# Optimization experiments

Hardware: AMD Instinct MI355X
Metric: run time of the kernel (lower is better)

Reference implementation:

```python
import jax, jax.numpy as jnp
import numpy as np

S, B, D, H, DFF = 1024, 8, 1024, 16, 4096
HD = D // H
EPS = 1e-5


def layernorm(x, g, b):
    m = jnp.mean(x, axis=-1, keepdims=True)
    v = jnp.mean(jnp.square(x - m), axis=-1, keepdims=True)
    return (x - m) * jax.lax.rsqrt(v + EPS) * g + b


def setup_inputs() -> dict:
    key = jax.random.key(0)
    ks = jax.random.split(key, 6)
    w = 0.02
    return {
        "src": jax.random.normal(ks[0], (S, B, D), dtype=jnp.float32),
        "in_proj_w": jax.random.normal(ks[1], (3 * D, D), dtype=jnp.float32) * w,
        "in_proj_b": jnp.zeros((3 * D,), dtype=jnp.float32),
        "out_w": jax.random.normal(ks[2], (D, D), dtype=jnp.float32) * w,
        "out_b": jnp.zeros((D,), dtype=jnp.float32),
        "lin1_w": jax.random.normal(ks[3], (DFF, D), dtype=jnp.float32) * w,
        "lin1_b": jnp.zeros((DFF,), dtype=jnp.float32),
        "lin2_w": jax.random.normal(ks[4], (D, DFF), dtype=jnp.float32) * w,
        "lin2_b": jnp.zeros((D,), dtype=jnp.float32),
        "n1_g": jnp.ones((D,), dtype=jnp.float32),
        "n1_b": jnp.zeros((D,), dtype=jnp.float32),
        "n2_g": jnp.ones((D,), dtype=jnp.float32),
        "n2_b": jnp.zeros((D,), dtype=jnp.float32),
    }


def reference(src, in_proj_w, in_proj_b, out_w, out_b,
              lin1_w, lin1_b, lin2_w, lin2_b,
              n1_g, n1_b, n2_g, n2_b):
    # self-attention block (eval mode: dropout = identity)
    qkv = jnp.einsum('sbd,ed->sbe', src, in_proj_w) + in_proj_b  # [S,B,3D]
    q, k, v = jnp.split(qkv, 3, axis=-1)
    q = q.reshape(S, B, H, HD) * (1.0 / np.sqrt(HD)).astype(np.float32)
    k = k.reshape(S, B, H, HD)
    v = v.reshape(S, B, H, HD)
    scores = jnp.einsum('sbhd,tbhd->bhst', q, k)        # [B,H,S,S]
    attn = jax.nn.softmax(scores, axis=-1)
    o = jnp.einsum('bhst,tbhd->sbhd', attn, v).reshape(S, B, D)
    o = jnp.einsum('sbd,ed->sbe', o, out_w) + out_b
    # post-LN residuals
    x = layernorm(src + o, n1_g, n1_b)
    h = jax.nn.relu(jnp.einsum('sbd,fd->sbf', x, lin1_w) + lin1_b)
    f = jnp.einsum('sbf,df->sbd', h, lin2_w) + lin2_b
    return layernorm(x + f, n2_g, n2_b)
```

## Files before the change

### kernel.cpp

```cpp
#include <hip/hip_runtime.h>
#include <cstdint>
#include <cstddef>

#define S_  1024
#define B_  8
#define D_  1024
#define H_  16
#define HD_ 64
#define DFF_ 4096
#define M_  (S_*B_)
#define QKV_N (3*D_)

typedef float f32x4 __attribute__((ext_vector_type(4)));
typedef __bf16 bf16x8 __attribute__((ext_vector_type(8)));
typedef __bf16 bf16x4 __attribute__((ext_vector_type(4)));

#define GLDS16(gp, lp) __builtin_amdgcn_global_load_lds( \
    (__attribute__((address_space(1))) void*)(gp), \
    (__attribute__((address_space(3))) void*)(lp), 16, 0, 0)

#define CB0 (M_*D_/4)
#define CB1 (CB0 + QKV_N*D_/4)
#define CB2 (CB1 + D_*D_/4)
#define CB3 (CB2 + DFF_*D_/4)
#define CB4 (CB3 + D_*DFF_/4)

__global__ __launch_bounds__(256)
void cvt_all(const float* __restrict__ src, const float* __restrict__ w1f,
             const float* __restrict__ w2f, const float* __restrict__ w3f,
             const float* __restrict__ w4f,
             __bf16* __restrict__ src_bf, __bf16* __restrict__ w1,
             __bf16* __restrict__ w2, __bf16* __restrict__ w3,
             __bf16* __restrict__ w4)
{
    int i = blockIdx.x * 256 + threadIdx.x;
    const float* in; __bf16* out; int off;
    if      (i < CB0) { in = src; out = src_bf; off = 0;   }
    else if (i < CB1) { in = w1f; out = w1;     off = CB0; }
    else if (i < CB2) { in = w2f; out = w2;     off = CB1; }
    else if (i < CB3) { in = w3f; out = w3;     off = CB2; }
    else if (i < CB4) { in = w4f; out = w4;     off = CB3; }
    else return;
    int j = i - off;
    float4 v = *(const float4*)(in + (size_t)j * 4);
    __bf16 t[4] = {(__bf16)v.x, (__bf16)v.y, (__bf16)v.z, (__bf16)v.w};
    *(uint2*)(out + (size_t)j * 4) = *(uint2*)t;
}

template<bool OUT_BF16, bool RELU, bool ADD_BIAS, bool SPLITZ>
__global__ __launch_bounds__(512, 2)
void gemm256(const __bf16* __restrict__ A, const __bf16* __restrict__ W,
             const float* __restrict__ bias,
             void* __restrict__ Cv0, void* __restrict__ Cv1,
             int N, int Kloop, int lda)
{
    extern __shared__ __bf16 lds[];

    const int tid  = threadIdx.x;
    const int lane = tid & 63;
    const int wv   = tid >> 6;
    const int quad = lane >> 4;
    const int l15  = lane & 15;
    const int wm   = (wv >> 2) * 128;
    const int wn   = (wv & 3) * 64;

    const int id  = blockIdx.y * gridDim.x + blockIdx.x;
    const int nwg = gridDim.x * gridDim.y;
    const int q8  = nwg >> 3;
    const int k   = (id & 7) * q8 + (id >> 3);
    const int within = k & 31;
    const int chunk  = k >> 5;
    const int nchm   = gridDim.x >> 3;
    const int cm     = chunk % nchm;
    const int cn     = chunk / nchm;
    const int m0 = (cm * 8 + (within & 7)) * 256;
    const int n0 = (cn * 4 + (within >> 3)) * 256;

    void* Cv = Cv0;
    if (SPLITZ) {
        const int koff = blockIdx.z * Kloop;
        A += koff;
        W += koff;
        if (blockIdx.z) Cv = Cv1;
    }

    const int nt = Kloop >> 5;

    const int crow = tid >> 2;
    const int csl  = (tid & 3) ^ ((crow >> 1) & 3);
    const __bf16* gA0 = A + (size_t)(m0 + crow) * lda + csl * 8;
    const __bf16* gA1 = gA0 + (size_t)128 * lda;
    const __bf16* gW0 = W + (size_t)(n0 + crow) * lda + csl * 8;
    const __bf16* gW1 = gW0 + (size_t)128 * lda;
    char* ldsSt = (char*)lds + tid * 16;

    #define STAGE(kt, buf) do { \
        const int ko = (kt) << 5; \
        char* d_ = ldsSt + (buf) * 32768; \
        GLDS16(gW0 + ko, d_ + 16384); \
        GLDS16(gW1 + ko, d_ + 24576); \
        GLDS16(gA0 + ko, d_); \
        GLDS16(gA1 + ko, d_ + 8192); \
    } while (0)

    const int swz = (quad ^ ((l15 >> 1) & 3)) * 8;
    const __bf16* aBase = lds + (wm + l15) * 32 + swz;
    const __bf16* bBase = lds + 8192 + (wn + l15) * 32 + swz;

    #define RDA_ALL(arr, buf) do { const __bf16* p_ = aBase + (buf) * 16384; \
        _Pragma("unroll") for (int i_ = 0; i_ < 8; ++i_) \
            arr[i_] = *(const bf16x8*)(p_ + i_ * 512); } while (0)
    #define RDB_ALL(arr, buf) do { const __bf16* p_ = bBase + (buf) * 16384; \
        _Pragma("unroll") for (int j_ = 0; j_ < 4; ++j_) \
            arr[j_] = *(const bf16x8*)(p_ + j_ * 512); } while (0)

    #define BARRIER_DRAIN() do { \
        asm volatile("s_waitcnt vmcnt(0)" ::: "memory"); \
        __builtin_amdgcn_s_barrier(); \
        __builtin_amdgcn_sched_barrier(0); \
    } while (0)

    STAGE(0, 0);
    STAGE(1, 1);
    BARRIER_DRAIN();

    f32x4 acc[8][4] = {};
    bf16x8 aP[8], aN[8], b_[4];

    RDA_ALL(aP, 0);

    int b_cur = 0;
    for (int t = 0; t < nt; t += 2) {
        int b_nxt = b_cur + 1; if (b_nxt == 3) b_nxt = 0;
        int b_st  = b_nxt + 1; if (b_st  == 3) b_st  = 0;

        if (t + 2 < nt) STAGE(t + 2, b_st);
        RDB_ALL(b_, b_cur);
        RDA_ALL(aN, b_nxt);
        __builtin_amdgcn_s_setprio(1);
        #pragma unroll
        for (int i = 0; i < 8; ++i)
            #pragma unroll
            for (int j = 0; j < 4; ++j)
                acc[i][j] = __builtin_amdgcn_mfma_f32_16x16x32_bf16(aP[i], b_[j], acc[i][j], 0, 0, 0);
        __builtin_amdgcn_s_setprio(0);
        BARRIER_DRAIN();

        if (t + 3 < nt) STAGE(t + 3, b_cur);
        RDB_ALL(b_, b_nxt);
        if (t + 2 < nt) RDA_ALL(aP, b_st);
        __builtin_amdgcn_s_setprio(1);
        #pragma unroll
        for (int i = 0; i < 8; ++i)
            #pragma unroll
            for (int j = 0; j < 4; ++j)
                acc[i][j] = __builtin_amdgcn_mfma_f32_16x16x32_bf16(aN[i], b_[j], acc[i][j], 0, 0, 0);
        __builtin_amdgcn_s_setprio(0);
        if (t + 2 < nt) BARRIER_DRAIN();

        b_cur = b_st;
    }

    #undef BARRIER_DRAIN
    #undef RDA_ALL
    #undef RDB_ALL
    #undef STAGE

    float bvj[4];
    #pragma unroll
    for (int j = 0; j < 4; ++j)
        bvj[j] = ADD_BIAS ? bias[n0 + wn + j * 16 + l15] : 0.f;
    const size_t cbase = (size_t)(m0 + wm + quad * 4) * N + (n0 + wn + l15);
    #pragma unroll
    for (int i = 0; i < 8; ++i) {
        #pragma unroll
        for (int r = 0; r < 4; ++r) {
            const size_t rowb = cbase + (size_t)(i * 16 + r) * N;
            #pragma unroll
            for (int j = 0; j < 4; ++j) {
                float v = acc[i][j][r] + bvj[j];
                if (RELU) v = fmaxf(v, 0.f);
                if (OUT_BF16)
                    ((__bf16*)Cv)[rowb + j * 16] = (__bf16)v;
                else
                    ((float*)Cv)[rowb + j * 16] = v;
            }
        }
    }
}

template<bool OUT_BF16, bool RELU, bool ADD_BIAS, bool SPLITZ>
__global__ __launch_bounds__(512, 4)
void gemm128(const __bf16* __restrict__ A, const __bf16* __restrict__ W,
             const float* __restrict__ bias,
             void* __restrict__ Cv0, void* __restrict__ Cv1,
             int N, int Kloop, int lda)
{
    extern __shared__ __bf16 lds[];

    const int tid  = threadIdx.x;
    const int lane = tid & 63;
    const int wv   = tid >> 6;
    const int quad = lane >> 4;
    const int l15  = lane & 15;
    const int wm   = (wv & 1) * 64;
    const int wn   = (wv >> 1) * 64;

    const int id  = blockIdx.y * gridDim.x + blockIdx.x;
    const int nwg = gridDim.x * gridDim.y;
    const int q8  = nwg >> 3;
    const int k   = (id & 7) * q8 + (id >> 3);
    const int within = k & 31;
    const int chunk  = k >> 5;
    const int nchm   = gridDim.x >> 3;
    const int cm     = chunk % nchm;
    const int cn     = chunk / nchm;
    const int m0 = (cm * 8 + (within & 7)) * 128;
    const int n0 = (cn * 4 + (within >> 3)) * 256;

    void* Cv = Cv0;
    if (SPLITZ) {
        const int koff = blockIdx.z * Kloop;
        A += koff;
        W += koff;
        if (blockIdx.z) Cv = Cv1;
    }

    const int nt = Kloop >> 5;

    const int crow = tid >> 2;
    const int csl  = (tid & 3) ^ ((crow >> 1) & 3);
    const __bf16* gA0 = A + (size_t)(m0 + crow) * lda + csl * 8;
    const __bf16* gW0 = W + (size_t)(n0 + crow) * lda + csl * 8;
    const __bf16* gW1 = gW0 + (size_t)128 * lda;
    char* ldsSt = (char*)lds + tid * 16;

    #define STAGE(kt, buf) do { \
        const int ko = (kt) << 5; \
        char* d_ = ldsSt + (buf) * 24576; \
        GLDS16(gW0 + ko, d_ + 8192); \
        GLDS16(gW1 + ko, d_ + 16384); \
        GLDS16(gA0 + ko, d_); \
    } while (0)

    const int swz = (quad ^ ((l15 >> 1) & 3)) * 8;
    const __bf16* aBase = lds + (wm + l15) * 32 + swz;
    const __bf16* bBase = lds + 4096 + (wn + l15) * 32 + swz;

    #define BARRIER_DRAIN() do { \
        asm volatile("s_waitcnt vmcnt(0)" ::: "memory"); \
        __builtin_amdgcn_s_barrier(); \
        __builtin_amdgcn_sched_barrier(0); \
    } while (0)

    STAGE(0, 0);
    BARRIER_DRAIN();

    f32x4 acc[4][4] = {};

    for (int t = 0; t < nt; ++t) {
        const int cur = t & 1;
        if (t + 1 < nt) STAGE(t + 1, cur ^ 1);

        const __bf16* aB = aBase + cur * 12288;
        const __bf16* bB = bBase + cur * 12288;
        bf16x8 b_[4];
        #pragma unroll
        for (int j = 0; j < 4; ++j)
            b_[j] = *(const bf16x8*)(bB + j * 512);
        __builtin_amdgcn_s_setprio(1);
        #pragma unroll
        for (int i = 0; i < 4; ++i) {
            bf16x8 a_ = *(const bf16x8*)(aB + i * 512);
            #pragma unroll
            for (int j = 0; j < 4; ++j)
                acc[i][j] = __builtin_amdgcn_mfma_f32_16x16x32_bf16(a_, b_[j], acc[i][j], 0, 0, 0);
        }
        __builtin_amdgcn_s_setprio(0);

        if (t + 1 < nt) BARRIER_DRAIN();
    }

    #undef BARRIER_DRAIN
    #undef STAGE

    float bvj[4];
    #pragma unroll
    for (int j = 0; j < 4; ++j)
        bvj[j] = ADD_BIAS ? bias[n0 + wn + j * 16 + l15] : 0.f;
    const size_t cbase = (size_t)(m0 + wm + quad * 4) * N + (n0 + wn + l15);
    #pragma unroll
    for (int i = 0; i < 4; ++i) {
        #pragma unroll
        for (int r = 0; r < 4; ++r) {
            const size_t rowb = cbase + (size_t)(i * 16 + r) * N;
            #pragma unroll
            for (int j = 0; j < 4; ++j) {
                float v = acc[i][j][r] + bvj[j];
                if (RELU) v = fmaxf(v, 0.f);
                if (OUT_BF16)
                    ((__bf16*)Cv)[rowb + j * 16] = (__bf16)v;
                else
                    ((float*)Cv)[rowb + j * 16] = v;
            }
        }
    }
}

__global__ __launch_bounds__(256)
void v_transpose(const __bf16* __restrict__ qkv, __bf16* __restrict__ vt)
{
    __shared__ __bf16 T[64 * 65];
    const int tid = threadIdx.x;
    const int t0  = blockIdx.x * 64;
    const int bh  = blockIdx.y;
    const int b   = bh & (B_ - 1);
    const int h   = bh / B_;

    #pragma unroll
    for (int j = 0; j < 2; ++j) {
        int c = j * 256 + tid;
        int i = c >> 3, cc = c & 7;
        const __bf16* g = qkv + (size_t)((t0 + i) * B_ + b) * QKV_N + 2 * D_ + h * HD_ + cc * 8;
        bf16x8 v = *(const bf16x8*)g;
        #pragma unroll
        for (int u = 0; u < 8; ++u) T[(cc * 8 + u) * 65 + i] = v[u];
    }
    __syncthreads();
    #pragma unroll
    for (int j = 0; j < 2; ++j) {
        int c = j * 256 + tid;
        int d = c >> 3, cc = c & 7;
        __bf16 pk[8];
        #pragma unroll
        for (int u = 0; u < 8; ++u) pk[u] = T[d * 65 + cc * 8 + u];
        *(uint4*)(vt + ((size_t)bh * HD_ + d) * S_ + t0 + cc * 8) = *(uint4*)pk;
    }
}

__global__ __launch_bounds__(512, 4)
void attn_flash(const __bf16* __restrict__ qkv, const __bf16* __restrict__ vt,
                __bf16* __restrict__ out)
{
    extern __shared__ __bf16 alds[];
    __bf16* Ks0 = alds;
    __bf16* Vs0 = alds + 16384;
    __bf16* Ps  = alds + 32768;

    const int tid  = threadIdx.x;
    const int lane = tid & 63;
    const int wv   = tid >> 6;
    const int quad = lane >> 4;
    const int l15  = lane & 15;

    const int id = blockIdx.y * gridDim.x + blockIdx.x;
    const int k  = (id & 7) * ((S_ / 128) * B_ * H_ / 8) + (id >> 3);
    const int s0 = (k & 7) * 128;
    const int bh = k >> 3;
    const int b  = bh & (B_ - 1);
    const int h  = bh / B_;

    const int i0k = tid >> 3, cck = tid & 7, scck = cck ^ (i0k & 7);
    const int i0v = tid >> 4, ccv = tid & 15, sccv = ccv ^ (i0v & 15);
    const __bf16* gK0 = qkv + ((size_t)i0k * B_ + b) * QKV_N + D_ + h * HD_ + scck * 8;
    const __bf16* gK1 = gK0 + (size_t)64 * B_ * QKV_N;
    const __bf16* gV0 = vt + ((size_t)bh * HD_ + i0v) * S_ + sccv * 8;
    const __bf16* gV1 = gV0 + (size_t)32 * S_;
    char* dK = (char*)Ks0 + tid * 16;
    char* dV = (char*)Vs0 + tid * 16;
    const size_t KADV = (size_t)128 * B_ * QKV_N;

    #define STAGEKV(buf) do { \
        GLDS16(gK0, dK + (buf) * 16384); \
        GLDS16(gK1, dK + (buf) * 16384 + 8192); \
        GLDS16(gV0, dV + (buf) * 16384); \
        GLDS16(gV1, dV + (buf) * 16384 + 8192); \
        gK0 += KADV; gK1 += KADV; gV0 += 128; gV1 += 128; \
    } while (0)

    STAGEKV(0);

    const int qrow = wv * 16 + l15;
    bf16x8 bq[2];
    #pragma unroll
    for (int kk = 0; kk < 2; ++kk)
        bq[kk] = *(const bf16x8*)(qkv + (size_t)((s0 + qrow) * B_ + b) * QKV_N
                                  + h * HD_ + kk * 32 + quad * 8);

    __syncthreads();

    f32x4 oacc[4] = {};
    float l_run = 0.f;
    const float C2 = 0.125f * 1.44269504f;
    const int xk = l15 & 7;
    const __bf16* psB = Ps + qrow * 64;

    const int nt2 = S_ / 128;
    for (int it = 0; it < nt2; ++it) {
        const int cur = it & 1;
        if (it + 1 < nt2) STAGEKV(cur ^ 1);

        #pragma unroll
        for (int s = 0; s < 2; ++s) {
            f32x4 sacc[4] = {};
            #pragma unroll
            for (int kk = 0; kk < 2; ++kk) {
                const __bf16* akB = Ks0 + cur * 8192 + s * 4096 + l15 * 64
                                    + (((kk * 4 + quad) ^ xk) * 8);
                #pragma unroll
                for (int j = 0; j < 4; ++j)
                    sacc[j] = __builtin_amdgcn_mfma_f32_16x16x32_bf16(
                        *(const bf16x8*)(akB + j * 1024), bq[kk], sacc[j], 0, 0, 0);
            }

            float rs = 0.f;
            #pragma unroll
            for (int j = 0; j < 4; ++j)
                #pragma unroll
                for (int r = 0; r < 4; ++r) {
                    float p = __builtin_amdgcn_exp2f(sacc[j][r] * C2);
                    sacc[j][r] = p;
                    rs += p;
                }
            rs += __shfl_xor(rs, 16, 64);
            rs += __shfl_xor(rs, 32, 64);
            l_run += rs;

            #pragma unroll
            for (int j = 0; j < 4; ++j) {
                __bf16 pk[4] = {(__bf16)sacc[j][0], (__bf16)sacc[j][1],
                                (__bf16)sacc[j][2], (__bf16)sacc[j][3]};
                int s16 = (j * 2 + (quad >> 1)) ^ xk;
                *(uint2*)(psB + s16 * 8 + (quad & 1) * 4) = *(uint2*)pk;
            }

            #pragma unroll
            for (int kk = 0; kk < 2; ++kk) {
                bf16x8 ap = *(const bf16x8*)(psB + (((kk * 4 + quad) ^ xk) * 8));
                const __bf16* bvB = Vs0 + cur * 8192 + l15 * 128
                                    + (((s * 8 + kk * 4 + quad) ^ l15) * 8);
                #pragma unroll
                for (int jd = 0; jd < 4; ++jd)
                    oacc[jd] = __builtin_amdgcn_mfma_f32_16x16x32_bf16(
                        ap, *(const bf16x8*)(bvB + jd * 2048), oacc[jd], 0, 0, 0);
            }
        }

        __syncthreads();
    }
    #undef STAGEKV

    float linv = 1.f / l_run;
    #pragma unroll
    for (int r = 0; r < 4; ++r) {
        float lr = __shfl(linv, quad * 4 + r, 64);
        int s = s0 + wv * 16 + quad * 4 + r;
        #pragma unroll
        for (int jd = 0; jd < 4; ++jd) {
            int d = jd * 16 + l15;
            out[(size_t)(s * B_ + b) * D_ + h * HD_ + d] = (__bf16)(oacc[jd][r] * lr);
        }
    }
}

__global__ __launch_bounds__(256)
void ln_res3(const float* __restrict__ xa, const __bf16* __restrict__ p0,
             const __bf16* __restrict__ p1, const float* __restrict__ bias,
             const float* __restrict__ g, const float* __restrict__ beta,
             float* __restrict__ yout, __bf16* __restrict__ ybf)
{
    __shared__ float red[8];
    const int row = blockIdx.x;
    const int tid = threadIdx.x;
    const size_t base = (size_t)row * D_ + tid * 4;

    float4 a  = *(const float4*)(xa + base);
    bf16x4 q0 = *(const bf16x4*)(p0 + base);
    bf16x4 q1 = *(const bf16x4*)(p1 + base);
    float4 bb = *(const float4*)(bias + tid * 4);
    float x0 = a.x + (float)q0[0] + (float)q1[0] + bb.x;
    float x1 = a.y + (float)q0[1] + (float)q1[1] + bb.y;
    float x2 = a.z + (float)q0[2] + (float)q1[2] + bb.z;
    float x3 = a.w + (float)q0[3] + (float)q1[3] + bb.w;

    float s  = x0 + x1 + x2 + x3;
    float ss = x0 * x0 + x1 * x1 + x2 * x2 + x3 * x3;
    for (int msk = 1; msk <= 32; msk <<= 1) {
        s  += __shfl_xor(s,  msk, 64);
        ss += __shfl_xor(ss, msk, 64);
    }
    const int wv = tid >> 6;
    if ((tid & 63) == 0) { red[wv] = s; red[4 + wv] = ss; }
    __syncthreads();
    s  = red[0] + red[1] + red[2] + red[3];
    ss = red[4] + red[5] + red[6] + red[7];
    float mean = s * (1.f / D_);
    float var  = ss * (1.f / D_) - mean * mean;
    float rstd = rsqrtf(var + 1e-5f);

    float4 gv = *(const float4*)(g + tid * 4);
    float4 bv = *(const float4*)(beta + tid * 4);
    float y0 = (x0 - mean) * rstd * gv.x + bv.x;
    float y1 = (x1 - mean) * rstd * gv.y + bv.y;
    float y2 = (x2 - mean) * rstd * gv.z + bv.z;
    float y3 = (x3 - mean) * rstd * gv.w + bv.w;
    *(float4*)(yout + base) = make_float4(y0, y1, y2, y3);
    if (ybf) {
        __bf16 t[4] = {(__bf16)y0, (__bf16)y1, (__bf16)y2, (__bf16)y3};
        *(uint2*)(ybf + base) = *(uint2*)t;
    }
}

extern "C" void kernel_launch(void* const* d_in, const int* in_sizes, int n_in,
                              void* d_out, int out_size, void* d_ws, size_t ws_size,
                              hipStream_t stream)
{
    const float* src       = (const float*)d_in[0];
    const float* in_proj_w = (const float*)d_in[1];
    const float* in_proj_b = (const float*)d_in[2];
    const float* out_w     = (const float*)d_in[3];
    const float* out_b     = (const float*)d_in[4];
    const float* lin1_w    = (const float*)d_in[5];
    const float* lin1_b    = (const float*)d_in[6];
    const float* lin2_w    = (const float*)d_in[7];
    const float* lin2_b    = (const float*)d_in[8];
    const float* n1_g = (const float*)d_in[9];
    const float* n1_b = (const float*)d_in[10];
    const float* n2_g = (const float*)d_in[11];
    const float* n2_b = (const float*)d_in[12];

    char* ws = (char*)d_ws;
    size_t off = 0;
    auto alloc = [&](size_t bytes) { char* p = ws + off; off += (bytes + 255) & ~(size_t)255; return p; };

    __bf16* src_bf = (__bf16*)alloc((size_t)M_ * D_ * 2);
    __bf16* w1     = (__bf16*)alloc((size_t)QKV_N * D_ * 2);
    __bf16* w2     = (__bf16*)alloc((size_t)D_ * D_ * 2);
    __bf16* w3     = (__bf16*)alloc((size_t)DFF_ * D_ * 2);
    __bf16* w4     = (__bf16*)alloc((size_t)D_ * DFF_ * 2);
    __bf16* qkv    = (__bf16*)alloc((size_t)M_ * QKV_N * 2);
    char*   h_r    = alloc((size_t)M_ * DFF_ * 2);
    __bf16* xbf    = (__bf16*)alloc((size_t)M_ * D_ * 2);
    float*  xf     = (float*)alloc((size_t)M_ * D_ * 4);
    __bf16* vt     = (__bf16*)alloc((size_t)B_ * H_ * HD_ * S_ * 2);

    const size_t PART = (size_t)M_ * D_;
    __bf16* attn_o = src_bf;
    __bf16* o0 = (__bf16*)h_r;
    __bf16* o1 = o0 + PART;
    __bf16* hbf = (__bf16*)h_r;
    __bf16* f0 = vt;
    __bf16* f1 = xbf;

    const size_t SHM   = 98304;
    const size_t SHM2  = 49152;
    const size_t ASHM  = 81920;

    cvt_all<<<(CB4 + 255) / 256, 256, 0, stream>>>(
        src, in_proj_w, out_w, lin1_w, lin2_w, src_bf, w1, w2, w3, w4);

    gemm128<true, false, true, false><<<dim3(M_ / 128, QKV_N / 256), 512, SHM2, stream>>>(
        src_bf, w1, in_proj_b, qkv, nullptr, QKV_N, D_, D_);

    v_transpose<<<dim3(S_ / 64, B_ * H_), 256, 0, stream>>>(qkv, vt);

    attn_flash<<<dim3(S_ / 128, B_ * H_), 512, ASHM, stream>>>(qkv, vt, attn_o);

    gemm256<true, false, false, true><<<dim3(M_ / 256, D_ / 256, 2), 512, SHM, stream>>>(
        attn_o, w2, nullptr, o0, o1, D_, D_ / 2, D_);

    ln_res3<<<M_, 256, 0, stream>>>(src, o0, o1, out_b, n1_g, n1_b, xf, xbf);

    gemm256<true, true, true, false><<<dim3(M_ / 256, DFF_ / 256), 512, SHM, stream>>>(
        xbf, w3, lin1_b, hbf, nullptr, DFF_, D_, D_);

    gemm256<true, false, false, true><<<dim3(M_ / 256, D_ / 256, 2), 512, SHM, stream>>>(
        hbf, w4, nullptr, f0, f1, D_, DFF_ / 2, DFF_);

    ln_res3<<<M_, 256, 0, stream>>>(xf, f0, f1, lin2_b, n2_g, n2_b, (float*)d_out, nullptr);
}
```

Measured before the change: 443.7 us.

## Rework 256x256 GEMM into 8-phase pipeline with 64-wide K tiles and finer prefetch

Replaces the triple-buffered 32-wide K loop with a double-buffered 64-wide K tile. Each tile is split into four barrier-separated phases that interleave LDS reads, partial global-to-LDS prefetches and 16-MFMA bursts, with hand-tuned vmcnt waits. The goal is to hide global load latency and spread LDS traffic evenly across MFMA work instead of draining all loads at each barrier. It raises LDS use to 128KB per block, which may limit occupancy to one block per CU, and adds many more barriers.

Measured after the change: 451.0 us. Within noise of the previous version (+1.7%).

```diff
diff --git a/kernel.cpp b/kernel.cpp
--- a/kernel.cpp
+++ b/kernel.cpp
@@ -49,10 +49,10 @@
 
 template<bool OUT_BF16, bool RELU, bool ADD_BIAS, bool SPLITZ>
 __global__ __launch_bounds__(512, 2)
-void gemm256(const __bf16* __restrict__ A, const __bf16* __restrict__ W,
-             const float* __restrict__ bias,
-             void* __restrict__ Cv0, void* __restrict__ Cv1,
-             int N, int Kloop, int lda)
+void gemm8p(const __bf16* __restrict__ A, const __bf16* __restrict__ W,
+            const float* __restrict__ bias,
+            void* __restrict__ Cv0, void* __restrict__ Cv1,
+            int N, int Kloop, int lda)
 {
     extern __shared__ __bf16 lds[];
 
@@ -84,87 +84,95 @@
         if (blockIdx.z) Cv = Cv1;
     }
 
-    const int nt = Kloop >> 5;
+    const int nt = Kloop >> 6;
 
     const int crow = tid >> 2;
     const int csl  = (tid & 3) ^ ((crow >> 1) & 3);
-    const __bf16* gA0 = A + (size_t)(m0 + crow) * lda + csl * 8;
-    const __bf16* gA1 = gA0 + (size_t)128 * lda;
-    const __bf16* gW0 = W + (size_t)(n0 + crow) * lda + csl * 8;
-    const __bf16* gW1 = gW0 + (size_t)128 * lda;
+    const __bf16* gA[2] = { A + (size_t)(m0 + crow) * lda + csl * 8,
+                            A + (size_t)(m0 + 128 + crow) * lda + csl * 8 };
+    const __bf16* gW[2] = { W + (size_t)(n0 + crow) * lda + csl * 8,
+                            W + (size_t)(n0 + 128 + crow) * lda + csl * 8 };
     char* ldsSt = (char*)lds + tid * 16;
 
-    #define STAGE(kt, buf) do { \
-        const int ko = (kt) << 5; \
-        char* d_ = ldsSt + (buf) * 32768; \
-        GLDS16(gW0 + ko, d_ + 16384); \
-        GLDS16(gW1 + ko, d_ + 24576); \
-        GLDS16(gA0 + ko, d_); \
-        GLDS16(gA1 + ko, d_ + 8192); \
+    #define CHA(kv, hh, kt) GLDS16(gA[hh] + ((kt) << 6) + (kv) * 32, \
+        ldsSt + (((kt) & 1) * 65536 + (kv) * 16384 + (hh) * 8192))
+    #define CHB(kv, hh, kt) GLDS16(gW[hh] + ((kt) << 6) + (kv) * 32, \
+        ldsSt + (((kt) & 1) * 65536 + 32768 + (kv) * 16384 + (hh) * 8192))
+
+    const int swzE = (quad ^ ((l15 >> 1) & 3)) * 8;
+    const __bf16* aBase = lds + (wm + l15) * 32 + swzE;
+    const __bf16* bBase = lds + 16384 + (wn + l15) * 32 + swzE;
+
+    CHB(0,0,0); CHB(0,1,0); CHA(0,0,0); CHA(0,1,0);
+    CHB(1,0,0); CHB(1,1,0); CHA(1,0,0); CHA(1,1,0);
+    CHB(0,0,1); CHB(0,1,1); CHA(0,0,1); CHA(0,1,1);
+    CHB(1,0,1); CHB(1,1,1);
+    asm volatile("s_waitcnt vmcnt(6)" ::: "memory");
+    __builtin_amdgcn_s_barrier();
+
+    f32x4 acc[8][4] = {};
+
+    #define KTILE(T, S1, S2, VM1, VM2) do { \
+        const __bf16* aB = aBase + ((T) & 1) * 32768; \
+        const __bf16* bB = bBase + ((T) & 1) * 32768; \
+        bf16x8 b_[4], a_[4]; \
+         \
+        _Pragma("unroll") for (int j = 0; j < 4; ++j) b_[j] = *(const bf16x8*)(bB + j * 512); \
+        _Pragma("unroll") for (int i = 0; i < 4; ++i) a_[i] = *(const bf16x8*)(aB + i * 512); \
+        if (S1) { CHA(1,0,(T)+1); CHA(1,1,(T)+1); } \
+        __builtin_amdgcn_s_barrier(); \
+        asm volatile("s_waitcnt lgkmcnt(0)" ::: "memory"); \
+        __builtin_amdgcn_s_setprio(1); \
+        _Pragma("unroll") for (int i = 0; i < 4; ++i) \
+            _Pragma("unroll") for (int j = 0; j < 4; ++j) \
+                acc[i][j] = __builtin_amdgcn_mfma_f32_16x16x32_bf16(a_[i], b_[j], acc[i][j], 0, 0, 0); \
+        __builtin_amdgcn_s_setprio(0); \
+        __builtin_amdgcn_s_barrier(); \
+         \
+        _Pragma("unroll") for (int i = 0; i < 4; ++i) a_[i] = *(const bf16x8*)(aB + (i + 4) * 512); \
+        if (S2) { CHB(0,0,(T)+2); CHB(0,1,(T)+2); } \
+        __builtin_amdgcn_s_barrier(); \
+        asm volatile("s_waitcnt lgkmcnt(0)" ::: "memory"); \
+        __builtin_amdgcn_s_setprio(1); \
+        _Pragma("unroll") for (int i = 0; i < 4; ++i) \
+            _Pragma("unroll") for (int j = 0; j < 4; ++j) \
+                acc[i+4][j] = __builtin_amdgcn_mfma_f32_16x16x32_bf16(a_[i], b_[j], acc[i+4][j], 0, 0, 0); \
+        __builtin_amdgcn_s_setprio(0); \
+        asm volatile("s_waitcnt vmcnt(" VM1 ")" ::: "memory"); \
+        __builtin_amdgcn_s_barrier(); \
+         \
+        _Pragma("unroll") for (int j = 0; j < 4; ++j) b_[j] = *(const bf16x8*)(bB + 8192 + j * 512); \
+        _Pragma("unroll") for (int i = 0; i < 4; ++i) a_[i] = *(const bf16x8*)(aB + 8192 + i * 512); \
+        if (S2) { CHA(0,0,(T)+2); CHA(0,1,(T)+2); } \
+        __builtin_amdgcn_s_barrier(); \
+        asm volatile("s_waitcnt lgkmcnt(0)" ::: "memory"); \
+        __builtin_amdgcn_s_setprio(1); \
+        _Pragma("unroll") for (int i = 0; i < 4; ++i) \
+            _Pragma("unroll") for (int j = 0; j < 4; ++j) \
+                acc[i][j] = __builtin_amdgcn_mfma_f32_16x16x32_bf16(a_[i], b_[j], acc[i][j], 0, 0, 0); \
+        __builtin_amdgcn_s_setprio(0); \
+        __builtin_amdgcn_s_barrier(); \
+         \
+        _Pragma("unroll") for (int i = 0; i < 4; ++i) a_[i] = *(const bf16x8*)(aB + 8192 + (i + 4) * 512); \
+        if (S2) { CHB(1,0,(T)+2); CHB(1,1,(T)+2); } \
+        __builtin_amdgcn_s_barrier(); \
+        asm volatile("s_waitcnt lgkmcnt(0)" ::: "memory"); \
+        __builtin_amdgcn_s_setprio(1); \
+        _Pragma("unroll") for (int i = 0; i < 4; ++i) \
+            _Pragma("unroll") for (int j = 0; j < 4; ++j) \
+                acc[i+4][j] = __builtin_amdgcn_mfma_f32_16x16x32_bf16(a_[i], b_[j], acc[i+4][j], 0, 0, 0); \
+        __builtin_amdgcn_s_setprio(0); \
+        asm volatile("s_waitcnt vmcnt(" VM2 ")" ::: "memory"); \
+        __builtin_amdgcn_s_barrier(); \
     } while (0)
 
-    const int swz = (quad ^ ((l15 >> 1) & 3)) * 8;
-    const __bf16* aBase = lds + (wm + l15) * 32 + swz;
-    const __bf16* bBase = lds + 8192 + (wn + l15) * 32 + swz;
-
-    #define RDA_ALL(arr, buf) do { const __bf16* p_ = aBase + (buf) * 16384; \
-        _Pragma("unroll") for (int i_ = 0; i_ < 8; ++i_) \
-            arr[i_] = *(const bf16x8*)(p_ + i_ * 512); } while (0)
-    #define RDB_ALL(arr, buf) do { const __bf16* p_ = bBase + (buf) * 16384; \
-        _Pragma("unroll") for (int j_ = 0; j_ < 4; ++j_) \
-            arr[j_] = *(const bf16x8*)(p_ + j_ * 512); } while (0)
-
-    #define BARRIER_DRAIN() do { \
-        asm volatile("s_waitcnt vmcnt(0)" ::: "memory"); \
-        __builtin_amdgcn_s_barrier(); \
-        __builtin_amdgcn_sched_barrier(0); \
-    } while (0)
-
-    STAGE(0, 0);
-    STAGE(1, 1);
-    BARRIER_DRAIN();
-
-    f32x4 acc[8][4] = {};
-    bf16x8 aP[8], aN[8], b_[4];
-
-    RDA_ALL(aP, 0);
-
-    int b_cur = 0;
-    for (int t = 0; t < nt; t += 2) {
-        int b_nxt = b_cur + 1; if (b_nxt == 3) b_nxt = 0;
-        int b_st  = b_nxt + 1; if (b_st  == 3) b_st  = 0;
-
-        if (t + 2 < nt) STAGE(t + 2, b_st);
-        RDB_ALL(b_, b_cur);
-        RDA_ALL(aN, b_nxt);
-        __builtin_amdgcn_s_setprio(1);
-        #pragma unroll
-        for (int i = 0; i < 8; ++i)
-            #pragma unroll
-            for (int j = 0; j < 4; ++j)
-                acc[i][j] = __builtin_amdgcn_mfma_f32_16x16x32_bf16(aP[i], b_[j], acc[i][j], 0, 0, 0);
-        __builtin_amdgcn_s_setprio(0);
-        BARRIER_DRAIN();
-
-        if (t + 3 < nt) STAGE(t + 3, b_cur);
-        RDB_ALL(b_, b_nxt);
-        if (t + 2 < nt) RDA_ALL(aP, b_st);
-        __builtin_amdgcn_s_setprio(1);
-        #pragma unroll
-        for (int i = 0; i < 8; ++i)
-            #pragma unroll
-            for (int j = 0; j < 4; ++j)
-                acc[i][j] = __builtin_amdgcn_mfma_f32_16x16x32_bf16(aN[i], b_[j], acc[i][j], 0, 0, 0);
-        __builtin_amdgcn_s_setprio(0);
-        if (t + 2 < nt) BARRIER_DRAIN();
-
-        b_cur = b_st;
-    }
-
-    #undef BARRIER_DRAIN
-    #undef RDA_ALL
-    #undef RDB_ALL
-    #undef STAGE
+    for (int t = 0; t < nt - 2; ++t) KTILE(t, true, true, "10", "10");
+    KTILE(nt - 2, true,  false, "8", "4");
+    KTILE(nt - 1, false, false, "0", "0");
+
+    #undef KTILE
+    #undef CHA
+    #undef CHB
 
     float bvj[4];
     #pragma unroll
@@ -552,7 +560,7 @@
     __bf16* f0 = vt;
     __bf16* f1 = xbf;
 
-    const size_t SHM   = 98304;
+    const size_t SHM8  = 131072;
     const size_t SHM2  = 49152;
     const size_t ASHM  = 81920;
 
@@ -566,15 +574,15 @@
 
     attn_flash<<<dim3(S_ / 128, B_ * H_), 512, ASHM, stream>>>(qkv, vt, attn_o);
 
-    gemm256<true, false, false, true><<<dim3(M_ / 256, D_ / 256, 2), 512, SHM, stream>>>(
+    gemm8p<true, false, false, true><<<dim3(M_ / 256, D_ / 256, 2), 512, SHM8, stream>>>(
         attn_o, w2, nullptr, o0, o1, D_, D_ / 2, D_);
 
     ln_res3<<<M_, 256, 0, stream>>>(src, o0, o1, out_b, n1_g, n1_b, xf, xbf);
 
-    gemm256<true, true, true, false><<<dim3(M_ / 256, DFF_ / 256), 512, SHM, stream>>>(
+    gemm8p<true, true, true, false><<<dim3(M_ / 256, DFF_ / 256), 512, SHM8, stream>>>(
         xbf, w3, lin1_b, hbf, nullptr, DFF_, D_, D_);
 
-    gemm256<true, false, false, true><<<dim3(M_ / 256, D_ / 256, 2), 512, SHM, stream>>>(
+    gemm8p<true, false, false, true><<<dim3(M_ / 256, D_ / 256, 2), 512, SHM8, stream>>>(
         hbf, w4, nullptr, f0, f1, D_, DFF_ / 2, DFF_);
 
     ln_res3<<<M_, 256, 0, stream>>>(xf, f0, f1, lin2_b, n2_g, n2_b, (float*)d_out, nullptr);
```
